# Optimization experiments

Measured on AMD Instinct MI355X. Metric: run time of the kernel, lower is better.

The kernel has to match this reference:

```python
import jax, jax.numpy as jnp
import numpy as np

B, D, R, P, N, PR = 128, 1024, 36, 8, 16, 4
MARGIN = 0.0
N_O, N_A, N_R, N_C = 0.5, 0.5, 0.5, 0.5


def setup_inputs() -> dict:
    key = jax.random.key(0)
    ks = jax.random.split(key, 12)
    return {
        "img_emb": jax.random.normal(ks[0], (B, D), jnp.float32),
        "sent_emb": jax.random.normal(ks[1], (B, D), jnp.float32),
        "comp_emb": jax.random.normal(ks[2], (B, D), jnp.float32),
        "img_feat_emb": jax.random.normal(ks[3], (B, R, D), jnp.float32),
        "obj_emb": jax.random.normal(ks[4], (B, P, D), jnp.float32),
        "neg_obj_emb": jax.random.normal(ks[5], (B, P, N, D), jnp.float32),
        "attr_emb": jax.random.normal(ks[6], (B, P, D), jnp.float32),
        "neg_attr_n_emb": jax.random.normal(ks[7], (B, P, N, D), jnp.float32),
        "neg_attr_a_emb": jax.random.normal(ks[8], (B, P, N, D), jnp.float32),
        "rel_emb": jax.random.normal(ks[9], (B, PR, D), jnp.float32),
        "neg_rel_emb": jax.random.normal(ks[10], (B, PR, N, D), jnp.float32),
        "rel_idx": jax.random.randint(ks[11], (B,), 0, PR, jnp.int64 if jax.config.jax_enable_x64 else jnp.int32),
    }


def contrastive(im, s, unidirectional=False):
    # cosine_sim: im @ s.T; hinge vs diagonal, diagonal masked out
    scores = im @ s.T                      # [B,B]
    diag = jnp.diagonal(scores)
    off = 1.0 - jnp.eye(scores.shape[0], dtype=scores.dtype)
    cost_s = jnp.maximum(MARGIN + scores - diag[:, None], 0.0) * off
    cost_im = jnp.maximum(MARGIN + scores - diag[None, :], 0.0) * off
    if unidirectional:
        return cost_s.sum()
    return cost_s.sum() + cost_im.sum()


def global_loss(img_feats, pos, neg):
    # Eq.1: per positive embedding, hinge vs hardest negative (max over N)
    pos_sim = jnp.einsum("bpd,bd->bp", pos, img_feats)          # [B,P]
    neg_sim = jnp.einsum("bpnd,bd->bpn", neg, img_feats)        # [B,P,N]
    max_neg = neg_sim.max(axis=2)                                # [B,P]
    return jnp.maximum(MARGIN + max_neg - pos_sim, 0.0).sum()


def local_loss(img_feats, pos, neg):
    # Eq.2/3: attention-weighted hinge over regions
    sims = jnp.einsum("bpd,brd->bpr", pos, img_feats)            # [B,P,R]
    m = jax.nn.softmax(sims, axis=2)
    neg_sims = jnp.einsum("bpnd,brd->bpnr", neg, img_feats)      # [B,P,N,R]
    max_neg = neg_sims.max(axis=2)                               # [B,P,R]
    return (m * jnp.maximum(MARGIN + max_neg - sims, 0.0)).sum()


def reference(img_emb, sent_emb, comp_emb, img_feat_emb, obj_emb, neg_obj_emb,
              attr_emb, neg_attr_n_emb, neg_attr_a_emb, rel_emb, neg_rel_emb,
              rel_idx):
    l_sent = contrastive(img_emb, sent_emb)
    l_comp = contrastive(img_emb, comp_emb)
    l_obj = local_loss(img_feat_emb, obj_emb, neg_obj_emb)
    l_attr = (local_loss(img_feat_emb, attr_emb, neg_attr_n_emb)
              + local_loss(img_feat_emb, attr_emb, neg_attr_a_emb))
    rel_samp = rel_emb[jnp.arange(rel_emb.shape[0]), rel_idx]    # [B,D]
    l_rel = (contrastive(img_emb, rel_samp, unidirectional=True)
             + global_loss(img_emb, rel_emb, neg_rel_emb))
    total = l_sent + N_C * l_comp + N_R * l_rel + N_A * l_attr + N_O * l_obj
    others = jnp.stack([l_obj, l_attr, l_rel, l_comp, l_sent])
    return total, others
```

## Files before the change

kernel.cpp:

```cpp
#include <hip/hip_runtime.h>

#define BB   128
#define DD   1024
#define RR   36
#define PP   8
#define NNEG 16
#define PRR  4

typedef __bf16 bf16x8 __attribute__((ext_vector_type(8)));
typedef float f32x4 __attribute__((ext_vector_type(4)));

#define WS_DIAG 16
#define WSF_OFF_BYTES 4096
#define WSF_PER_B (3 * 32 * 64 * 8)
#define WSF_BYTES ((size_t)WSF_OFF_BYTES + (size_t)BB * WSF_PER_B * 2)

__global__ __launch_bounds__(64) void k_zero(float* __restrict__ ws) {
    int t = threadIdx.x;
    if (t < 8) ws[t] = 0.0f;
}

__global__ __launch_bounds__(64) void k_diag(const float* __restrict__ img,
                                             const float* __restrict__ sent,
                                             const float* __restrict__ comp,
                                             const float* __restrict__ rel,
                                             const int*   __restrict__ relidx,
                                             float* __restrict__ ws) {
    const int i = blockIdx.x, t = blockIdx.y, lane = threadIdx.x;
    const float* x;
    if (t == 0)      x = sent + (size_t)i * DD;
    else if (t == 1) x = comp + (size_t)i * DD;
    else             x = rel + ((size_t)i * PRR + relidx[i]) * DD;
    const float* a = img + (size_t)i * DD;
    float acc = 0.0f;
#pragma unroll
    for (int k = 0; k < 4; ++k) {
        float4 va = *reinterpret_cast<const float4*>(a + lane * 4 + k * 256);
        float4 vb = *reinterpret_cast<const float4*>(x + lane * 4 + k * 256);
        acc += va.x * vb.x + va.y * vb.y + va.z * vb.z + va.w * vb.w;
    }
#pragma unroll
    for (int off = 32; off > 0; off >>= 1) acc += __shfl_down(acc, off);
    if (lane == 0) ws[WS_DIAG + t * BB + i] = acc;
}

__global__ __launch_bounds__(256) void k_contrastive(const float* __restrict__ img,
                                                     const float* __restrict__ sent,
                                                     const float* __restrict__ comp,
                                                     const float* __restrict__ rel,
                                                     const int*   __restrict__ relidx,
                                                     float* __restrict__ ws) {
    const int t  = blockIdx.z;
    const int i0 = blockIdx.y * 16, j0 = blockIdx.x * 16;
    const int tid = threadIdx.x, ty = tid >> 4, tx = tid & 15;
    __shared__ float As[16][68];
    __shared__ float Bs[16][68];
    __shared__ float red[4];

    const int j_row = j0 + ty;
    const float* brow;
    if (t == 0)      brow = sent + (size_t)j_row * DD;
    else if (t == 1) brow = comp + (size_t)j_row * DD;
    else             brow = rel + ((size_t)j_row * PRR + relidx[j_row]) * DD;
    const float* arow = img + (size_t)(i0 + ty) * DD;

    float acc = 0.0f;
    for (int kc = 0; kc < DD; kc += 64) {
        __syncthreads();
        float4 va = *reinterpret_cast<const float4*>(arow + kc + tx * 4);
        float4 vb = *reinterpret_cast<const float4*>(brow + kc + tx * 4);
        *reinterpret_cast<float4*>(&As[ty][tx * 4]) = va;
        *reinterpret_cast<float4*>(&Bs[ty][tx * 4]) = vb;
        __syncthreads();
#pragma unroll 8
        for (int d = 0; d < 64; ++d)
            acc += As[ty][d] * Bs[tx][d];
    }

    const int i = i0 + ty, j = j0 + tx;
    const float diag_i = ws[WS_DIAG + t * BB + i];
    const float diag_j = ws[WS_DIAG + t * BB + j];
    float contrib = 0.0f;
    if (i != j) {
        contrib = fmaxf(acc - diag_i, 0.0f);
        if (t < 2) contrib += fmaxf(acc - diag_j, 0.0f);
    }
#pragma unroll
    for (int off = 32; off > 0; off >>= 1) contrib += __shfl_down(contrib, off);
    if ((tid & 63) == 0) red[tid >> 6] = contrib;
    __syncthreads();
    if (tid == 0) {
        const int slot = (t == 0) ? 4 : (t == 1) ? 3 : 2;
        atomicAdd(&ws[slot], red[0] + red[1] + red[2] + red[3]);
    }
}

__global__ __launch_bounds__(64) void k_globalrel(const float* __restrict__ img,
                                                  const float* __restrict__ rel,
                                                  const float* __restrict__ negrel,
                                                  float* __restrict__ ws) {
    const int blk = blockIdx.x, b = blk >> 2, p = blk & 3;
    const int lane = threadIdx.x;
    const float* a = img + (size_t)b * DD;
    float4 ir[4];
#pragma unroll
    for (int k = 0; k < 4; ++k)
        ir[k] = *reinterpret_cast<const float4*>(a + lane * 4 + k * 256);

    auto dotv = [&](const float* __restrict__ v) -> float {
        float acc = 0.0f;
#pragma unroll
        for (int k = 0; k < 4; ++k) {
            float4 w = *reinterpret_cast<const float4*>(v + lane * 4 + k * 256);
            acc += ir[k].x * w.x + ir[k].y * w.y + ir[k].z * w.z + ir[k].w * w.w;
        }
#pragma unroll
        for (int off = 32; off > 0; off >>= 1) acc += __shfl_xor(acc, off);
        return acc;
    };

    float pos = dotv(rel + ((size_t)b * PRR + p) * DD);
    float mx = -1e30f;
    const float* nb = negrel + ((size_t)b * PRR + p) * NNEG * DD;
    for (int n = 0; n < NNEG; ++n) mx = fmaxf(mx, dotv(nb + (size_t)n * DD));
    if (lane == 0) atomicAdd(&ws[2], fmaxf(mx - pos, 0.0f));
}

__global__ __launch_bounds__(256) void k_featcvt(const float* __restrict__ feat,
                                                 __bf16* __restrict__ wsf) {
    const int b = blockIdx.x, nt = blockIdx.y, tid = threadIdx.x;
    const float* fb = feat + (size_t)b * RR * DD;
    __bf16* ob = wsf + (size_t)b * WSF_PER_B + (size_t)nt * 32 * 64 * 8;
    for (int i = tid; i < 32 * 64; i += 256) {
        const int ks = i >> 6, lane = i & 63;
        const int r = nt * 16 + (lane & 15);
        const int k0 = ks * 32 + (lane >> 4) * 8;
        bf16x8 w;
        if (r < RR) {
            float4 v0 = *reinterpret_cast<const float4*>(fb + (size_t)r * DD + k0);
            float4 v1 = *reinterpret_cast<const float4*>(fb + (size_t)r * DD + k0 + 4);
            w[0] = (__bf16)v0.x; w[1] = (__bf16)v0.y; w[2] = (__bf16)v0.z; w[3] = (__bf16)v0.w;
            w[4] = (__bf16)v1.x; w[5] = (__bf16)v1.y; w[6] = (__bf16)v1.z; w[7] = (__bf16)v1.w;
        } else {
#pragma unroll
            for (int j = 0; j < 8; ++j) w[j] = (__bf16)0.0f;
        }
        *reinterpret_cast<bf16x8*>(ob + (size_t)i * 8) = w;
    }
}

template <bool WSFEAT>
__global__ __launch_bounds__(256) void k_local3(const float* __restrict__ feat,
                                                const float* __restrict__ obj,
                                                const float* __restrict__ attr,
                                                const float* __restrict__ nobj,
                                                const float* __restrict__ nattrn,
                                                const float* __restrict__ nattra,
                                                const __bf16* __restrict__ wsf,
                                                float* __restrict__ ws) {
    const int t = blockIdx.x;
    const int b = blockIdx.y;
    const int tid = threadIdx.x;
    const int wv = tid >> 6;
    const int p = blockIdx.z * 4 + wv;
    const int lane = tid & 63;
    const int lrow = lane & 15;
    const int kgq = lane >> 4;

    const float* pos = (t == 0) ? obj : attr;
    const float* neg = (t == 0) ? nobj : (t == 1) ? nattrn : nattra;
    const float* posb = pos + ((size_t)b * PP + p) * DD + kgq * 8;
    const float* negb = neg + ((size_t)(b * PP + p) * NNEG + lrow) * DD + kgq * 8;
    const float* fb   = feat + (size_t)b * RR * DD;
    const __bf16* wfb = wsf + (size_t)b * WSF_PER_B + (size_t)lane * 8;

    f32x4 accn[3], accp[3];
#pragma unroll
    for (int nt = 0; nt < 3; ++nt) {
        accn[nt] = (f32x4){0.f, 0.f, 0.f, 0.f};
        accp[nt] = (f32x4){0.f, 0.f, 0.f, 0.f};
    }

    auto LOAD = [&](int ks, float4& n0, float4& n1, float4& p0, float4& p1, bf16x8* f) {
        const float* np = negb + ks * 32;
        n0 = *reinterpret_cast<const float4*>(np);
        n1 = *reinterpret_cast<const float4*>(np + 4);
        const float* pp = posb + ks * 32;
        p0 = *reinterpret_cast<const float4*>(pp);
        p1 = *reinterpret_cast<const float4*>(pp + 4);
        if (WSFEAT) {
#pragma unroll
            for (int nt = 0; nt < 3; ++nt)
                f[nt] = *reinterpret_cast<const bf16x8*>(wfb + ((size_t)(nt * 32 + ks)) * 512);
        } else {
#pragma unroll
            for (int nt = 0; nt < 3; ++nt) {
                const int r = nt * 16 + lrow;
                if (r < RR) {
                    const float* fp = fb + (size_t)r * DD + ks * 32 + kgq * 8;
                    float4 v0 = *reinterpret_cast<const float4*>(fp);
                    float4 v1 = *reinterpret_cast<const float4*>(fp + 4);
                    f[nt][0] = (__bf16)v0.x; f[nt][1] = (__bf16)v0.y;
                    f[nt][2] = (__bf16)v0.z; f[nt][3] = (__bf16)v0.w;
                    f[nt][4] = (__bf16)v1.x; f[nt][5] = (__bf16)v1.y;
                    f[nt][6] = (__bf16)v1.z; f[nt][7] = (__bf16)v1.w;
                } else {
#pragma unroll
                    for (int j = 0; j < 8; ++j) f[nt][j] = (__bf16)0.0f;
                }
            }
        }
    };

    float4 cn0, cn1, cp0, cp1;
    bf16x8 cf[3];
    LOAD(0, cn0, cn1, cp0, cp1, cf);

#pragma unroll
    for (int ks = 0; ks < 32; ++ks) {
        float4 nn0 = cn0, nn1 = cn1, np0 = cp0, np1 = cp1;
        bf16x8 nf[3] = {cf[0], cf[1], cf[2]};
        if (ks + 1 < 32) LOAD(ks + 1, nn0, nn1, np0, np1, nf);

        bf16x8 an, ap;
        an[0] = (__bf16)cn0.x; an[1] = (__bf16)cn0.y; an[2] = (__bf16)cn0.z; an[3] = (__bf16)cn0.w;
        an[4] = (__bf16)cn1.x; an[5] = (__bf16)cn1.y; an[6] = (__bf16)cn1.z; an[7] = (__bf16)cn1.w;
        ap[0] = (__bf16)cp0.x; ap[1] = (__bf16)cp0.y; ap[2] = (__bf16)cp0.z; ap[3] = (__bf16)cp0.w;
        ap[4] = (__bf16)cp1.x; ap[5] = (__bf16)cp1.y; ap[6] = (__bf16)cp1.z; ap[7] = (__bf16)cp1.w;

#pragma unroll
        for (int nt = 0; nt < 3; ++nt) {
            accn[nt] = __builtin_amdgcn_mfma_f32_16x16x32_bf16(an, cf[nt], accn[nt], 0, 0, 0);
            accp[nt] = __builtin_amdgcn_mfma_f32_16x16x32_bf16(ap, cf[nt], accp[nt], 0, 0, 0);
        }
        cn0 = nn0; cn1 = nn1; cp0 = np0; cp1 = np1;
        cf[0] = nf[0]; cf[1] = nf[1]; cf[2] = nf[2];
    }

    float s3[3], h3[3];
#pragma unroll
    for (int nt = 0; nt < 3; ++nt) {
        f32x4 a = accn[nt];
        float m = fmaxf(fmaxf(a[0], a[1]), fmaxf(a[2], a[3]));
        m = fmaxf(m, __shfl_xor(m, 16));
        m = fmaxf(m, __shfl_xor(m, 32));
        float s = accp[nt][0];
        s3[nt] = s;
        h3[nt] = fmaxf(m - s, 0.0f);
    }
    float mx = -1e30f;
#pragma unroll
    for (int nt = 0; nt < 3; ++nt)
        if (nt * 16 + lrow < RR) mx = fmaxf(mx, s3[nt]);
#pragma unroll
    for (int off = 1; off < 16; off <<= 1) mx = fmaxf(mx, __shfl_xor(mx, off));
    float den = 0.0f, num = 0.0f;
#pragma unroll
    for (int nt = 0; nt < 3; ++nt)
        if (nt * 16 + lrow < RR) {
            float e = __expf(s3[nt] - mx);
            den += e;
            num += e * h3[nt];
        }
#pragma unroll
    for (int off = 1; off < 16; off <<= 1) {
        den += __shfl_xor(den, off);
        num += __shfl_xor(num, off);
    }

    __shared__ float red[4];
    if (lane == 0) red[wv] = num / den;
    __syncthreads();
    if (tid == 0)
        atomicAdd(&ws[(t == 0) ? 0 : 1], red[0] + red[1] + red[2] + red[3]);
}

__global__ __launch_bounds__(64) void k_final(const float* __restrict__ ws,
                                              float* __restrict__ out) {
    if (threadIdx.x == 0) {
        const float obj = ws[0], attr = ws[1], rel = ws[2], comp = ws[3], sent = ws[4];
        out[0] = sent + 0.5f * comp + 0.5f * rel + 0.5f * attr + 0.5f * obj;
        out[1] = obj;
        out[2] = attr;
        out[3] = rel;
        out[4] = comp;
        out[5] = sent;
    }
}

extern "C" void kernel_launch(void* const* d_in, const int* in_sizes, int n_in,
                              void* d_out, int out_size, void* d_ws, size_t ws_size,
                              hipStream_t stream) {
    const float* img    = (const float*)d_in[0];
    const float* sent   = (const float*)d_in[1];
    const float* comp   = (const float*)d_in[2];
    const float* feat   = (const float*)d_in[3];
    const float* obj    = (const float*)d_in[4];
    const float* nobj   = (const float*)d_in[5];
    const float* attr   = (const float*)d_in[6];
    const float* nattrn = (const float*)d_in[7];
    const float* nattra = (const float*)d_in[8];
    const float* rel    = (const float*)d_in[9];
    const float* nrel   = (const float*)d_in[10];
    const int*   relidx = (const int*)d_in[11];
    float* ws  = (float*)d_ws;
    float* out = (float*)d_out;
    __bf16* wsf = (__bf16*)((char*)d_ws + WSF_OFF_BYTES);

    const bool usewsf = (ws_size >= WSF_BYTES);

    k_zero<<<dim3(1), dim3(64), 0, stream>>>(ws);
    k_diag<<<dim3(BB, 3), dim3(64), 0, stream>>>(img, sent, comp, rel, relidx, ws);
    k_contrastive<<<dim3(8, 8, 3), dim3(256), 0, stream>>>(img, sent, comp, rel, relidx, ws);
    k_globalrel<<<dim3(BB * PRR), dim3(64), 0, stream>>>(img, rel, nrel, ws);
    if (usewsf) {
        k_featcvt<<<dim3(BB, 3), dim3(256), 0, stream>>>(feat, wsf);
        k_local3<true><<<dim3(3, BB, 2), dim3(256), 0, stream>>>(feat, obj, attr, nobj, nattrn,
                                                                 nattra, wsf, ws);
    } else {
        k_local3<false><<<dim3(3, BB, 2), dim3(256), 0, stream>>>(feat, obj, attr, nobj, nattrn,
                                                                  nattra, wsf, ws);
    }
    k_final<<<dim3(1), dim3(64), 0, stream>>>(ws, out);
}
```

Measured before the change: 100.4 us.

## Split local-loss K dimension across two waves with shared-memory reduction

Each block now handles two p values, with two waves per p that each cover half of the D dimension. The partial MFMA accumulators are combined through shared memory before the softmax and hinge epilogue. The grid doubles along z, so the number of waves stays the same but each wave's serial K loop is half as long. This is meant to shorten per-wave latency and expose more memory parallelism, at the cost of an extra LDS exchange and barrier and of half the waves sitting idle during the epilogue.

```diff
diff --git a/kernel.cpp b/kernel.cpp
--- a/kernel.cpp
+++ b/kernel.cpp
@@ -150,7 +150,7 @@
 }
 
 template <bool WSFEAT>
-__global__ __launch_bounds__(256) void k_local3(const float* __restrict__ feat,
+__global__ __launch_bounds__(256) void k_local5(const float* __restrict__ feat,
                                                 const float* __restrict__ obj,
                                                 const float* __restrict__ attr,
                                                 const float* __restrict__ nobj,
@@ -162,10 +162,13 @@
     const int b = blockIdx.y;
     const int tid = threadIdx.x;
     const int wv = tid >> 6;
-    const int p = blockIdx.z * 4 + wv;
+    const int pp = wv >> 1;
+    const int kh = wv & 1;
+    const int p = blockIdx.z * 2 + pp;
     const int lane = tid & 63;
     const int lrow = lane & 15;
     const int kgq = lane >> 4;
+    const int ksbase = kh * 16;
 
     const float* pos = (t == 0) ? obj : attr;
     const float* neg = (t == 0) ? nobj : (t == 1) ? nattrn : nattra;
@@ -181,13 +184,14 @@
         accp[nt] = (f32x4){0.f, 0.f, 0.f, 0.f};
     }
 
-    auto LOAD = [&](int ks, float4& n0, float4& n1, float4& p0, float4& p1, bf16x8* f) {
+    auto LOAD = [&](int ksl, float4& n0, float4& n1, float4& p0, float4& p1, bf16x8* f) {
+        const int ks = ksbase + ksl;
         const float* np = negb + ks * 32;
         n0 = *reinterpret_cast<const float4*>(np);
         n1 = *reinterpret_cast<const float4*>(np + 4);
-        const float* pp = posb + ks * 32;
-        p0 = *reinterpret_cast<const float4*>(pp);
-        p1 = *reinterpret_cast<const float4*>(pp + 4);
+        const float* pp_ = posb + ks * 32;
+        p0 = *reinterpret_cast<const float4*>(pp_);
+        p1 = *reinterpret_cast<const float4*>(pp_ + 4);
         if (WSFEAT) {
 #pragma unroll
             for (int nt = 0; nt < 3; ++nt)
@@ -217,10 +221,10 @@
     LOAD(0, cn0, cn1, cp0, cp1, cf);
 
 #pragma unroll
-    for (int ks = 0; ks < 32; ++ks) {
+    for (int ksl = 0; ksl < 16; ++ksl) {
         float4 nn0 = cn0, nn1 = cn1, np0 = cp0, np1 = cp1;
         bf16x8 nf[3] = {cf[0], cf[1], cf[2]};
-        if (ks + 1 < 32) LOAD(ks + 1, nn0, nn1, np0, np1, nf);
+        if (ksl + 1 < 16) LOAD(ksl + 1, nn0, nn1, np0, np1, nf);
 
         bf16x8 an, ap;
         an[0] = (__bf16)cn0.x; an[1] = (__bf16)cn0.y; an[2] = (__bf16)cn0.z; an[3] = (__bf16)cn0.w;
@@ -237,42 +241,64 @@
         cf[0] = nf[0]; cf[1] = nf[1]; cf[2] = nf[2];
     }
 
-    float s3[3], h3[3];
-#pragma unroll
-    for (int nt = 0; nt < 3; ++nt) {
-        f32x4 a = accn[nt];
-        float m = fmaxf(fmaxf(a[0], a[1]), fmaxf(a[2], a[3]));
-        m = fmaxf(m, __shfl_xor(m, 16));
-        m = fmaxf(m, __shfl_xor(m, 32));
-        float s = accp[nt][0];
-        s3[nt] = s;
-        h3[nt] = fmaxf(m - s, 0.0f);
-    }
-    float mx = -1e30f;
-#pragma unroll
-    for (int nt = 0; nt < 3; ++nt)
-        if (nt * 16 + lrow < RR) mx = fmaxf(mx, s3[nt]);
-#pragma unroll
-    for (int off = 1; off < 16; off <<= 1) mx = fmaxf(mx, __shfl_xor(mx, off));
-    float den = 0.0f, num = 0.0f;
-#pragma unroll
-    for (int nt = 0; nt < 3; ++nt)
-        if (nt * 16 + lrow < RR) {
-            float e = __expf(s3[nt] - mx);
-            den += e;
-            num += e * h3[nt];
-        }
-#pragma unroll
-    for (int off = 1; off < 16; off <<= 1) {
-        den += __shfl_xor(den, off);
-        num += __shfl_xor(num, off);
-    }
-
-    __shared__ float red[4];
-    if (lane == 0) red[wv] = num / den;
+    __shared__ float X[2][64][17];
+    __shared__ float red[2];
+    if (kh == 1) {
+#pragma unroll
+        for (int nt = 0; nt < 3; ++nt) {
+            X[pp][lane][nt * 4 + 0] = accn[nt][0];
+            X[pp][lane][nt * 4 + 1] = accn[nt][1];
+            X[pp][lane][nt * 4 + 2] = accn[nt][2];
+            X[pp][lane][nt * 4 + 3] = accn[nt][3];
+            X[pp][lane][12 + nt]    = accp[nt][0];
+        }
+    }
+    __syncthreads();
+    if (kh == 0) {
+#pragma unroll
+        for (int nt = 0; nt < 3; ++nt) {
+            accn[nt][0] += X[pp][lane][nt * 4 + 0];
+            accn[nt][1] += X[pp][lane][nt * 4 + 1];
+            accn[nt][2] += X[pp][lane][nt * 4 + 2];
+            accn[nt][3] += X[pp][lane][nt * 4 + 3];
+            accp[nt][0] += X[pp][lane][12 + nt];
+        }
+
+        float s3[3], h3[3];
+#pragma unroll
+        for (int nt = 0; nt < 3; ++nt) {
+            f32x4 a = accn[nt];
+            float m = fmaxf(fmaxf(a[0], a[1]), fmaxf(a[2], a[3]));
+            m = fmaxf(m, __shfl_xor(m, 16));
+            m = fmaxf(m, __shfl_xor(m, 32));
+            float s = accp[nt][0];
+            s3[nt] = s;
+            h3[nt] = fmaxf(m - s, 0.0f);
+        }
+        float mx = -1e30f;
+#pragma unroll
+        for (int nt = 0; nt < 3; ++nt)
+            if (nt * 16 + lrow < RR) mx = fmaxf(mx, s3[nt]);
+#pragma unroll
+        for (int off = 1; off < 16; off <<= 1) mx = fmaxf(mx, __shfl_xor(mx, off));
+        float den = 0.0f, num = 0.0f;
+#pragma unroll
+        for (int nt = 0; nt < 3; ++nt)
+            if (nt * 16 + lrow < RR) {
+                float e = __expf(s3[nt] - mx);
+                den += e;
+                num += e * h3[nt];
+            }
+#pragma unroll
+        for (int off = 1; off < 16; off <<= 1) {
+            den += __shfl_xor(den, off);
+            num += __shfl_xor(num, off);
+        }
+        if (lane == 0) red[pp] = num / den;
+    }
     __syncthreads();
     if (tid == 0)
-        atomicAdd(&ws[(t == 0) ? 0 : 1], red[0] + red[1] + red[2] + red[3]);
+        atomicAdd(&ws[(t == 0) ? 0 : 1], red[0] + red[1]);
 }
 
 __global__ __launch_bounds__(64) void k_final(const float* __restrict__ ws,
@@ -315,10 +341,10 @@
     k_globalrel<<<dim3(BB * PRR), dim3(64), 0, stream>>>(img, rel, nrel, ws);
     if (usewsf) {
         k_featcvt<<<dim3(BB, 3), dim3(256), 0, stream>>>(feat, wsf);
-        k_local3<true><<<dim3(3, BB, 2), dim3(256), 0, stream>>>(feat, obj, attr, nobj, nattrn,
+        k_local5<true><<<dim3(3, BB, 4), dim3(256), 0, stream>>>(feat, obj, attr, nobj, nattrn,
                                                                  nattra, wsf, ws);
     } else {
-        k_local3<false><<<dim3(3, BB, 2), dim3(256), 0, stream>>>(feat, obj, attr, nobj, nattrn,
+        k_local5<false><<<dim3(3, BB, 4), dim3(256), 0, stream>>>(feat, obj, attr, nobj, nattrn,
                                                                   nattra, wsf, ws);
     }
     k_final<<<dim3(1), dim3(64), 0, stream>>>(ws, out);
```

Result: slower. 106.5 us (+6.1%).
